# Performance work log

Hardware: AMD Instinct MI355X
Metric: run time of the kernel (lower is better)

Reference implementation:

```python
import jax, jax.numpy as jnp
import numpy as np

B, V, D, E, F, H, HD = 16, 1024, 16, 64, 16, 128, 64
GRAPH_LAYERS, FLOW_ITERS, DUAL_ITERS = 2, 10, 10
STEP, MOM, BIG = 0.01, 0.9, 1e9


def _build_graph():
    # circulant graph: node v's d-th out-neighbor is v + offs[d] (mod V); offsets paired (o, -o)
    offs = np.array([1, -1, 2, -2, 3, -3, 4, -4, 5, -5, 6, -6, 7, -7, 8, -8], dtype=np.int32)
    v = np.arange(V, dtype=np.int32)[:, None]
    d = np.broadcast_to(np.arange(D, dtype=np.int32)[None, :], (V, D))
    adj = ((v + offs[None, :]) % V).astype(np.int32)
    inv_adj = ((v - offs[None, :]) % V).astype(np.int32)
    in_idx = np.stack([inv_adj, d], axis=-1)    # d-th incoming edge of v == out-edge (inv_adj[v,d], slot d)
    rev_idx = np.stack([adj, d], axis=-1)       # out-edge (v,d) is the d-th incoming edge of adj[v,d]
    opp_idx = np.stack([adj, d ^ 1], axis=-1)   # opposite edge (w->v) is slot d^1 at w (paired offsets)
    bt = lambda x: jnp.asarray(np.broadcast_to(x[None], (B,) + x.shape).copy())
    return bt(adj), bt(inv_adj), bt(in_idx), bt(rev_idx), bt(opp_idx)


def setup_inputs() -> dict:
    key = jax.random.key(0)
    ks = jax.random.split(key, 16)
    adj_lst, inv_adj_lst, in_indices, rev_indices, opp_indices = _build_graph()
    rn = lambda k, shape, scale=1.0: jax.random.normal(k, shape, dtype=jnp.float32) * scale
    s = lambda fan: 1.0 / float(np.sqrt(fan))
    return {
        'demands': rn(ks[0], (B, V, 1)),
        'node_features': rn(ks[1], (B, V, F)),
        'edge_lengths': jax.random.uniform(ks[2], (B, V, D), dtype=jnp.float32),
        'norm_edge_lengths': jax.random.uniform(ks[3], (B, V, D), dtype=jnp.float32),
        'node_emb': rn(ks[4], (V, E)),
        'W_enc': rn(ks[5], (E + F, H), s(E + F)), 'b_enc': jnp.zeros((H,), jnp.float32),
        'W_gat': rn(ks[6], (H, H), s(H)), 'b_gat': jnp.zeros((H,), jnp.float32),
        'a_gat': rn(ks[7], (H,), s(H)),
        'W_gru_x': rn(ks[8], (H, 3 * H), s(H)), 'W_gru_h': rn(ks[9], (H, 3 * H), s(H)),
        'b_gru': jnp.zeros((3 * H,), jnp.float32),
        'W_dec1': rn(ks[10], (2 * H, HD), s(2 * H)), 'b_dec1': jnp.zeros((HD,), jnp.float32),
        'W_dec2': rn(ks[11], (HD, 1), s(HD)), 'b_dec2': jnp.zeros((1,), jnp.float32),
        'W_dual1': rn(ks[12], (H, HD), s(H)), 'b_dual1': jnp.zeros((HD,), jnp.float32),
        'W_dual2': rn(ks[13], (HD, 1), s(HD)), 'b_dual2': jnp.zeros((1,), jnp.float32),
        'adj_lst': adj_lst, 'inv_adj_lst': inv_adj_lst,
        'in_indices': in_indices, 'rev_indices': rev_indices, 'opp_indices': opp_indices,
        'num_nodes': jnp.full((B,), V, dtype=jnp.int32),
    }


def _gather_nodes(values, idx, valid):
    # masked_gather with set_zero=True: values (B,V,H), idx (B,V,D) -> (B,V,D,H)
    bb = jnp.arange(values.shape[0])[:, None, None]
    g = values[bb, jnp.clip(idx, 0, values.shape[1] - 1)]
    return g * valid[..., None]


def _gather_edges(x, idx):
    # gather_nd into a (B,V,D,...) tensor; idx (B,V,D,2) = (node, slot), batch implicit
    bb = jnp.arange(x.shape[0])[:, None, None]
    return x[bb, idx[..., 0], idx[..., 1]]


def _sparsemax(z):
    n = z.shape[-1]
    zs = jnp.sort(z, axis=-1)[..., ::-1]
    k = jnp.arange(1, n + 1, dtype=z.dtype)
    zc = jnp.cumsum(zs, axis=-1)
    support = (1.0 + k * zs) > zc
    kz = jnp.sum(support, axis=-1, keepdims=True)
    tau = (jnp.take_along_axis(zc, kz - 1, axis=-1) - 1.0) / kz.astype(z.dtype)
    return jnp.maximum(z - tau, 0.0)


def _forward(demands, node_features, edge_lengths, norm_edge_lengths, node_emb, W_enc, b_enc,
             W_gat, b_gat, a_gat, W_gru_x, W_gru_h, b_gru, W_dec1, b_dec1, W_dec2, b_dec2,
             W_dual1, b_dual1, W_dual2, b_dual2,
             adj_lst, inv_adj_lst, in_indices, rev_indices, opp_indices, num_nodes):
    f32 = jnp.float32
    # embedding lookup with max_norm=1
    nrm = jnp.linalg.norm(node_emb, axis=-1, keepdims=True)
    emb = node_emb / jnp.maximum(nrm, 1.0)
    emb_b = jnp.broadcast_to(emb[None], (demands.shape[0], V, E))
    node_enc = jnp.concatenate([emb_b, node_features], axis=-1) @ W_enc + b_enc   # (B,V,H)
    mask = (adj_lst == num_nodes[:, None, None]).astype(f32)                       # 1 = padded slot
    valid = 1.0 - mask
    initial = _gather_nodes(node_enc, adj_lst, valid)                              # (B,V,D,H)
    h = initial
    for _ in range(GRAPH_LAYERS):
        # DirectionalGAT: per-edge transform, masked attention over slots, directional regather
        t = jnp.tanh(h @ W_gat + b_gat)                                            # (B,V,D,H)
        logits = jnp.einsum('bvdh,h->bvd', t, a_gat) - BIG * mask
        attn = jax.nn.softmax(logits, axis=-1)
        node_msg = jnp.einsum('bvd,bvdh->bvh', attn, t)                            # (B,V,H)
        msg = _gather_nodes(node_msg, adj_lst, valid)
        x = jnp.tanh(msg + initial)
        # GRU cell, shared weights over all edge states
        gx = x @ W_gru_x + b_gru
        gh = h @ W_gru_h
        z = jax.nn.sigmoid(gx[..., :H] + gh[..., :H])
        r = jax.nn.sigmoid(gx[..., H:2 * H] + gh[..., H:2 * H])
        cand = jnp.tanh(gx[..., 2 * H:] + r * gh[..., 2 * H:])
        h = z * h + (1.0 - z) * cand
    # decoder over (encoding, encoding + opposite-edge encoding)
    comb = h + _gather_edges(h, opp_indices)
    dec_in = jnp.concatenate([h, comb], axis=-1)
    nw = (jnp.tanh(dec_in @ W_dec1 + b_dec1) @ W_dec2 + b_dec2)[..., 0]            # (B,V,D)
    # destination attention: normalize over incoming edges, map back to outgoing layout
    inv_mask = (inv_adj_lst == num_nodes[:, None, None]).astype(f32)
    in_w = _gather_edges(nw, in_indices)
    dest_attn = jax.nn.softmax(in_w - BIG * inv_mask, axis=-1)
    nw = _gather_edges(dest_attn, rev_indices)
    pred = nw - BIG * mask
    normalized = _sparsemax(pred) * valid
    # iterative proportional min-cost-flow solver
    def mcf_step(flow, _):
        inflow = jnp.sum(_gather_edges(flow, in_indices), axis=-1, keepdims=True)  # (B,V,1)
        return normalized * jax.nn.relu(inflow - demands), None
    flow, _ = jax.lax.scan(mcf_step, jnp.zeros_like(normalized), None, length=FLOW_ITERS)
    flow_cost = jnp.sum(flow * flow, axis=(1, 2))                                  # square cost fn
    # dual variables + dual flow (projected momentum gradient descent)
    node_states = jnp.sum(h, axis=2)                                               # (B,V,H)
    dual_vars = jax.nn.relu(jnp.tanh(node_states @ W_dual1 + b_dual1) @ W_dual2 + b_dual2)  # (B,V,1)
    dual = mask * dual_vars
    dual_tr = _gather_nodes(dual_vars, adj_lst, valid)[..., 0]
    dual_diff = dual_tr - dual                                                     # (B,V,D)
    def dual_step(carry, _):
        f, vel = carry
        grad = 2.0 * f + dual_diff                                                 # d/df [f^2 + dual_diff*f]
        vel = MOM * vel - STEP * grad
        f = jax.nn.relu(f + vel)
        return (f, vel), None
    (dual_flows, _), _ = jax.lax.scan(dual_step, (jnp.zeros_like(dual_diff), jnp.zeros_like(dual_diff)), None, length=DUAL_ITERS)
    dual_flows = dual_flows * valid
    dual_demand = jnp.sum(dual_vars * demands, axis=(1, 2))
    dual_cost = jnp.sum(dual_flows * dual_flows + dual_diff * dual_flows, axis=(1, 2)) - dual_demand
    return flow_cost - dual_cost                                                   # (B,) primal-dual gap loss


def reference(demands, node_features, edge_lengths, norm_edge_lengths, node_emb, W_enc, b_enc,
              W_gat, b_gat, a_gat, W_gru_x, W_gru_h, b_gru, W_dec1, b_dec1, W_dec2, b_dec2,
              W_dual1, b_dual1, W_dual2, b_dual2,
              adj_lst, inv_adj_lst, in_indices, rev_indices, opp_indices, num_nodes):
    return _forward(demands, node_features, edge_lengths, norm_edge_lengths, node_emb, W_enc, b_enc,
                    W_gat, b_gat, a_gat, W_gru_x, W_gru_h, b_gru, W_dec1, b_dec1, W_dec2, b_dec2,
                    W_dual1, b_dual1, W_dual2, b_dual2,
                    adj_lst, inv_adj_lst, in_indices, rev_indices, opp_indices, num_nodes)
```

## Files before the change

kernel.cpp:

```cpp
#include <hip/hip_runtime.h>
#include <hip/hip_bf16.h>

#define B 16
#define V 1024
#define D 16
#define E 64
#define F 16
#define H 128
#define HD 64
#define BV (B*V)
#define BVD (B*V*D)

#define OFF_HNB      0
#define OFF_NORM     (OFF_HNB + BV*H/2)
#define OFF_DV       (OFF_NORM + BVD)
#define OFF_WT       (OFF_DV + BV)
#define OFF_WTG      (OFF_WT + 65536)
#define OFF_WPQ      (OFF_WTG + 8192)
#define OFF_WU1T     (OFF_WPQ + 8192)
#define OFF_WENCT    (OFF_WU1T + 4096)

typedef __attribute__((ext_vector_type(8))) short bf16x8;
typedef __attribute__((ext_vector_type(4))) float f32x4;

__device__ __forceinline__ short f2bf(float f){
  __hip_bfloat16 b = __float2bfloat16(f);
  return *reinterpret_cast<short*>(&b);
}
__device__ __forceinline__ float bf2f(short s){
  __hip_bfloat16 b; *reinterpret_cast<short*>(&b) = s;
  return __bfloat162float(b);
}
__device__ __forceinline__ float frcp(float x){ return __builtin_amdgcn_rcpf(x); }
__device__ __forceinline__ float fsig(float x){ return frcp(1.f + __expf(-x)); }
__device__ __forceinline__ float ftanh(float x){
  float e = __expf(-2.f*fabsf(x));
  float r = (1.f - e)*frcp(1.f + e);
  return copysignf(r, x);
}

__global__ __launch_bounds__(256) void k_pre(const float* __restrict__ Wx, const float* __restrict__ Wh,
    const float* __restrict__ Wg, const float* __restrict__ W1, const float* __restrict__ Wu1,
    const float* __restrict__ Wenc,
    short* __restrict__ Wt, short* __restrict__ Wgt, short* __restrict__ Wpq,
    short* __restrict__ Wu1t, short* __restrict__ Wenct){
  int bid = blockIdx.x, tid = threadIdx.x;
  if (bid < 512){
    int n = bid, k = tid;
    int g = n >> 7, j = n & 127;
    float v;
    if (g == 0)      v = (k < 128) ? Wx[k*384 + j]       : Wh[(k-128)*384 + j];
    else if (g == 1) v = (k < 128) ? Wx[k*384 + 128 + j] : Wh[(k-128)*384 + 128 + j];
    else if (g == 2) v = (k < 128) ? Wx[k*384 + 256 + j] : 0.f;
    else             v = (k < 128) ? 0.f                 : Wh[(k-128)*384 + 256 + j];
    Wt[n*256 + k] = f2bf(v);
    return;
  }
  if (bid < 576){
    int idx = (bid-512)*256 + tid;
    int n = idx >> 7, k = idx & 127;
    Wgt[n*128 + k] = f2bf(Wg[k*128 + n]);
    return;
  }
  if (bid < 608){
    int idx = (bid-576)*256 + tid;
    int n = idx >> 7, k = idx & 127;
    float wb = W1[(k+128)*HD + n];
    float wa = W1[k*HD + n];
    Wpq[n*128 + k]      = f2bf(wa + wb);
    Wpq[(64+n)*128 + k] = f2bf(wb);
    return;
  }
  if (bid < 640){
    int idx = (bid-608)*256 + tid;
    int n = idx >> 7, k = idx & 127;
    Wu1t[n*128 + k] = f2bf(Wu1[k*HD + n]);
    return;
  }
  {
    int nn = (bid-640)*2 + (tid >> 7);
    int kk = tid & 127;
    if (kk < 96) Wenct[nn*96 + kk] = f2bf(kk < 80 ? Wenc[kk*128 + nn] : 0.f);
  }
}

__global__ __launch_bounds__(256) void k_mega(const float* __restrict__ emb, const float* __restrict__ nf,
    const short* __restrict__ Wenct, const float* __restrict__ benc, const int* __restrict__ adj,
    const short* __restrict__ Wgt, const float* __restrict__ bg, const float* __restrict__ ag,
    const short* __restrict__ Wt, const float* __restrict__ bgru, short* __restrict__ hout){
  __shared__ short NE[96][136];
  __shared__ short T[96][136];
  __shared__ short H1[80][136];
  __shared__ short X[80][136];
  __shared__ float Lp[4][96];
  __shared__ float Ls[96];
  __shared__ float nrmv[96];
  short (*As)[104] = reinterpret_cast<short(*)[104]>(&H1[0][0]);

  int tid = threadIdx.x;
  int blk = blockIdx.x;
  int b = blk >> 4;
  int n0 = (blk & 15) << 6;
  int w = tid >> 6, lane = tid & 63;
  int l15 = lane & 15, quad = lane >> 4;

  if (tid < 96){
    int v = (n0 - 16 + tid) & 1023;
    const float4* e4 = reinterpret_cast<const float4*>(&emb[v*E]);
    float ss = 0.f;
    #pragma unroll
    for (int q=0;q<16;q++){ float4 x = e4[q]; ss += x.x*x.x + x.y*x.y + x.z*x.z + x.w*x.w; }
    nrmv[tid] = frcp(fmaxf(sqrtf(ss), 1.f));
  }
  __syncthreads();
  for (int e=tid; e<96*16; e+=256){
    int r = e >> 4, q = e & 15;
    int v = (n0 - 16 + r) & 1023;
    float4 x = reinterpret_cast<const float4*>(&emb[v*E])[q];
    float iv = nrmv[r];
    short4 s; s.x=f2bf(x.x*iv); s.y=f2bf(x.y*iv); s.z=f2bf(x.z*iv); s.w=f2bf(x.w*iv);
    *reinterpret_cast<short4*>(&As[r][q*4]) = s;
  }
  for (int e=tid; e<96*4; e+=256){
    int r = e >> 2, q = e & 3;
    int m = (b<<10) + ((n0 - 16 + r) & 1023);
    float4 x = reinterpret_cast<const float4*>(&nf[(long)m*F])[q];
    short4 s; s.x=f2bf(x.x); s.y=f2bf(x.y); s.z=f2bf(x.z); s.w=f2bf(x.w);
    *reinterpret_cast<short4*>(&As[r][64 + q*4]) = s;
    short4 z; z.x=0; z.y=0; z.z=0; z.w=0;
    *reinterpret_cast<short4*>(&As[r][80 + q*4]) = z;
  }
  __syncthreads();
  {
    f32x4 acc[6][2];
    #pragma unroll
    for (int mt=0;mt<6;mt++)
      #pragma unroll
      for (int u=0;u<2;u++) acc[mt][u] = (f32x4){0.f,0.f,0.f,0.f};
    #pragma unroll
    for (int kc=0;kc<3;kc++){
      int k0 = kc*32;
      bf16x8 a[6];
      #pragma unroll
      for (int mt=0;mt<6;mt++)
        a[mt] = *reinterpret_cast<const bf16x8*>(&As[16*mt + l15][k0 + quad*8]);
      #pragma unroll
      for (int u=0;u<2;u++){
        bf16x8 bfr = *reinterpret_cast<const bf16x8*>(&Wenct[(32*w + 16*u + l15)*96 + k0 + quad*8]);
        #pragma unroll
        for (int mt=0;mt<6;mt++)
          acc[mt][u] = __builtin_amdgcn_mfma_f32_16x16x32_bf16(a[mt], bfr, acc[mt][u], 0,0,0);
      }
    }
    #pragma unroll
    for (int u=0;u<2;u++){
      int c = 32*w + 16*u + l15;
      float bb = benc[c];
      #pragma unroll
      for (int mt=0;mt<6;mt++)
        #pragma unroll
        for (int reg=0;reg<4;reg++)
          NE[16*mt + quad*4 + reg][c] = f2bf(acc[mt][u][reg] + bb);
    }
  }
  __syncthreads();
  {
    f32x4 acc[6][2];
    #pragma unroll
    for (int mt=0;mt<6;mt++)
      #pragma unroll
      for (int u=0;u<2;u++) acc[mt][u] = (f32x4){0.f,0.f,0.f,0.f};
    #pragma unroll
    for (int kc=0;kc<4;kc++){
      int k0 = kc*32;
      bf16x8 a[6];
      #pragma unroll
      for (int mt=0;mt<6;mt++)
        a[mt] = *reinterpret_cast<const bf16x8*>(&NE[16*mt + l15][k0 + quad*8]);
      #pragma unroll
      for (int u=0;u<2;u++){
        bf16x8 bfr = *reinterpret_cast<const bf16x8*>(&Wgt[(32*w + 16*u + l15)*128 + k0 + quad*8]);
        #pragma unroll
        for (int mt=0;mt<6;mt++)
          acc[mt][u] = __builtin_amdgcn_mfma_f32_16x16x32_bf16(a[mt], bfr, acc[mt][u], 0,0,0);
      }
    }
    float lp[6][4];
    #pragma unroll
    for (int mt=0;mt<6;mt++)
      #pragma unroll
      for (int reg=0;reg<4;reg++) lp[mt][reg] = 0.f;
    #pragma unroll
    for (int u=0;u<2;u++){
      int c = 32*w + 16*u + l15;
      float bgc = bg[c], agc = ag[c];
      #pragma unroll
      for (int mt=0;mt<6;mt++){
        #pragma unroll
        for (int reg=0;reg<4;reg++){
          float t = ftanh(acc[mt][u][reg] + bgc);
          T[16*mt + quad*4 + reg][c] = f2bf(t);
          lp[mt][reg] += t * agc;
        }
      }
    }
    #pragma unroll
    for (int mt=0;mt<6;mt++)
      #pragma unroll
      for (int reg=0;reg<4;reg++){
        lp[mt][reg] += __shfl_xor(lp[mt][reg], 1);
        lp[mt][reg] += __shfl_xor(lp[mt][reg], 2);
        lp[mt][reg] += __shfl_xor(lp[mt][reg], 4);
        lp[mt][reg] += __shfl_xor(lp[mt][reg], 8);
      }
    if (l15 == 0){
      #pragma unroll
      for (int mt=0;mt<6;mt++)
        #pragma unroll
        for (int reg=0;reg<4;reg++)
          Lp[w][16*mt + quad*4 + reg] = lp[mt][reg];
    }
  }
  __syncthreads();
  if (tid < 96) Ls[tid] = Lp[0][tid]+Lp[1][tid]+Lp[2][tid]+Lp[3][tid];
  __syncthreads();
  for (int e=tid; e<320; e+=256){
    int vl = e >> 2, seg = e & 3;
    int wg = (b<<10) + ((n0 - 8 + vl) & 1023);
    int li[16]; float at[16];
    float m = -1e30f;
    #pragma unroll
    for (int d=0; d<16; d++){
      int a = adj[wg*16 + d];
      li[d] = (a - n0 + 16) & 1023;
      m = fmaxf(m, Ls[li[d]]);
    }
    float s = 0.f;
    #pragma unroll
    for (int d=0; d<16; d++){ at[d] = __expf(Ls[li[d]] - m); s += at[d]; }
    float inv = frcp(s);
    #pragma unroll
    for (int d=0; d<16; d++) at[d] *= inv;
    #pragma unroll
    for (int c8=0; c8<4; c8++){
      int c = seg*32 + c8*8;
      float acc8[8] = {0,0,0,0,0,0,0,0};
      #pragma unroll 4
      for (int d=0; d<16; d++){
        bf16x8 tv = *reinterpret_cast<const bf16x8*>(&T[li[d]][c]);
        float a = at[d];
        #pragma unroll
        for (int q=0;q<8;q++) acc8[q] += a * bf2f(tv[q]);
      }
      bf16x8 nv = *reinterpret_cast<const bf16x8*>(&NE[vl + 8][c]);
      bf16x8 xv;
      #pragma unroll
      for (int q=0;q<8;q++) xv[q] = f2bf(ftanh(acc8[q] + bf2f(nv[q])));
      *reinterpret_cast<bf16x8*>(&X[vl][c]) = xv;
    }
  }
  __syncthreads();
  {
    f32x4 acc[5][4][2];
    #pragma unroll
    for (int mt=0;mt<5;mt++)
      #pragma unroll
      for (int g=0;g<4;g++)
        #pragma unroll
        for (int u=0;u<2;u++) acc[mt][g][u] = (f32x4){0.f,0.f,0.f,0.f};
    for (int k8=0;k8<8;k8++){
      int k0 = k8*32;
      int gg = (k8 < 4) ? 2 : 3;
      bf16x8 a[5];
      #pragma unroll
      for (int mt=0;mt<5;mt++){
        if (k8 < 4) a[mt] = *reinterpret_cast<const bf16x8*>(&X[16*mt + l15][k0 + quad*8]);
        else        a[mt] = *reinterpret_cast<const bf16x8*>(&NE[16*mt + l15 + 8][k0 - 128 + quad*8]);
      }
      bf16x8 bz[2], br[2], bc[2];
      #pragma unroll
      for (int u=0;u<2;u++){
        int ncol = 32*w + 16*u + l15;
        int koff = k0 + quad*8;
        bz[u] = *reinterpret_cast<const bf16x8*>(&Wt[(ncol      )*256 + koff]);
        br[u] = *reinterpret_cast<const bf16x8*>(&Wt[(ncol + 128)*256 + koff]);
        bc[u] = *reinterpret_cast<const bf16x8*>(&Wt[(ncol + gg*128)*256 + koff]);
      }
      #pragma unroll
      for (int mt=0;mt<5;mt++){
        #pragma unroll
        for (int u=0;u<2;u++){
          acc[mt][0][u]  = __builtin_amdgcn_mfma_f32_16x16x32_bf16(a[mt], bz[u], acc[mt][0][u], 0,0,0);
          acc[mt][1][u]  = __builtin_amdgcn_mfma_f32_16x16x32_bf16(a[mt], br[u], acc[mt][1][u], 0,0,0);
          acc[mt][gg][u] = __builtin_amdgcn_mfma_f32_16x16x32_bf16(a[mt], bc[u], acc[mt][gg][u], 0,0,0);
        }
      }
    }
    #pragma unroll
    for (int u=0;u<2;u++){
      int j = 32*w + 16*u + l15;
      float bjz = bgru[j], bjr = bgru[128 + j], bjc = bgru[256 + j];
      #pragma unroll
      for (int mt=0;mt<5;mt++){
        #pragma unroll
        for (int reg=0;reg<4;reg++){
          int rl = 16*mt + quad*4 + reg;
          float z = fsig(acc[mt][0][u][reg] + bjz);
          float r = fsig(acc[mt][1][u][reg] + bjr);
          float cand = ftanh(acc[mt][2][u][reg] + bjc + r*acc[mt][3][u][reg]);
          float ho = bf2f(NE[rl + 8][j]);
          H1[rl][j] = f2bf(z*ho + (1.f - z)*cand);
        }
      }
    }
  }
  __syncthreads();
  {
    f32x4 acc[5][2];
    #pragma unroll
    for (int mt=0;mt<5;mt++)
      #pragma unroll
      for (int u=0;u<2;u++) acc[mt][u] = (f32x4){0.f,0.f,0.f,0.f};
    #pragma unroll
    for (int kc=0;kc<4;kc++){
      int k0 = kc*32;
      bf16x8 a[5];
      #pragma unroll
      for (int mt=0;mt<5;mt++)
        a[mt] = *reinterpret_cast<const bf16x8*>(&H1[16*mt + l15][k0 + quad*8]);
      #pragma unroll
      for (int u=0;u<2;u++){
        bf16x8 bfr = *reinterpret_cast<const bf16x8*>(&Wgt[(32*w + 16*u + l15)*128 + k0 + quad*8]);
        #pragma unroll
        for (int mt=0;mt<5;mt++)
          acc[mt][u] = __builtin_amdgcn_mfma_f32_16x16x32_bf16(a[mt], bfr, acc[mt][u], 0,0,0);
      }
    }
    float lp[5][4];
    #pragma unroll
    for (int mt=0;mt<5;mt++)
      #pragma unroll
      for (int reg=0;reg<4;reg++) lp[mt][reg] = 0.f;
    #pragma unroll
    for (int u=0;u<2;u++){
      int c = 32*w + 16*u + l15;
      float bgc = bg[c], agc = ag[c];
      #pragma unroll
      for (int mt=0;mt<5;mt++){
        #pragma unroll
        for (int reg=0;reg<4;reg++){
          float t = ftanh(acc[mt][u][reg] + bgc);
          T[16*mt + quad*4 + reg][c] = f2bf(t);
          lp[mt][reg] += t * agc;
        }
      }
    }
    #pragma unroll
    for (int mt=0;mt<5;mt++)
      #pragma unroll
      for (int reg=0;reg<4;reg++){
        lp[mt][reg] += __shfl_xor(lp[mt][reg], 1);
        lp[mt][reg] += __shfl_xor(lp[mt][reg], 2);
        lp[mt][reg] += __shfl_xor(lp[mt][reg], 4);
        lp[mt][reg] += __shfl_xor(lp[mt][reg], 8);
      }
    if (l15 == 0){
      #pragma unroll
      for (int mt=0;mt<5;mt++)
        #pragma unroll
        for (int reg=0;reg<4;reg++)
          Lp[w][16*mt + quad*4 + reg] = lp[mt][reg];
    }
  }
  __syncthreads();
  if (tid < 80) Ls[tid] = Lp[0][tid]+Lp[1][tid]+Lp[2][tid]+Lp[3][tid];
  __syncthreads();
  {
    int vl = tid >> 2, seg = tid & 3;
    int vg = (b<<10) + n0 + vl;
    int li[16]; float at[16];
    float m = -1e30f;
    #pragma unroll
    for (int d=0; d<16; d++){
      int a = adj[vg*16 + d];
      li[d] = (a - n0 + 8) & 1023;
      m = fmaxf(m, Ls[li[d]]);
    }
    float s = 0.f;
    #pragma unroll
    for (int d=0; d<16; d++){ at[d] = __expf(Ls[li[d]] - m); s += at[d]; }
    float inv = frcp(s);
    #pragma unroll
    for (int d=0; d<16; d++) at[d] *= inv;
    #pragma unroll
    for (int c8=0; c8<4; c8++){
      int c = seg*32 + c8*8;
      float acc8[8] = {0,0,0,0,0,0,0,0};
      #pragma unroll 4
      for (int d=0; d<16; d++){
        bf16x8 tv = *reinterpret_cast<const bf16x8*>(&T[li[d]][c]);
        float a = at[d];
        #pragma unroll
        for (int q=0;q<8;q++) acc8[q] += a * bf2f(tv[q]);
      }
      bf16x8 nv = *reinterpret_cast<const bf16x8*>(&NE[vl + 16][c]);
      bf16x8 xv;
      #pragma unroll
      for (int q=0;q<8;q++) xv[q] = f2bf(ftanh(acc8[q] + bf2f(nv[q])));
      *reinterpret_cast<bf16x8*>(&X[vl][c]) = xv;
    }
  }
  __syncthreads();
  {
    f32x4 acc[4][4][2];
    #pragma unroll
    for (int mt=0;mt<4;mt++)
      #pragma unroll
      for (int g=0;g<4;g++)
        #pragma unroll
        for (int u=0;u<2;u++) acc[mt][g][u] = (f32x4){0.f,0.f,0.f,0.f};
    for (int k8=0;k8<8;k8++){
      int k0 = k8*32;
      int gg = (k8 < 4) ? 2 : 3;
      bf16x8 a[4];
      #pragma unroll
      for (int mt=0;mt<4;mt++){
        if (k8 < 4) a[mt] = *reinterpret_cast<const bf16x8*>(&X[16*mt + l15][k0 + quad*8]);
        else        a[mt] = *reinterpret_cast<const bf16x8*>(&H1[16*mt + l15 + 8][k0 - 128 + quad*8]);
      }
      bf16x8 bz[2], br[2], bc[2];
      #pragma unroll
      for (int u=0;u<2;u++){
        int ncol = 32*w + 16*u + l15;
        int koff = k0 + quad*8;
        bz[u] = *reinterpret_cast<const bf16x8*>(&Wt[(ncol      )*256 + koff]);
        br[u] = *reinterpret_cast<const bf16x8*>(&Wt[(ncol + 128)*256 + koff]);
        bc[u] = *reinterpret_cast<const bf16x8*>(&Wt[(ncol + gg*128)*256 + koff]);
      }
      #pragma unroll
      for (int mt=0;mt<4;mt++){
        #pragma unroll
        for (int u=0;u<2;u++){
          acc[mt][0][u]  = __builtin_amdgcn_mfma_f32_16x16x32_bf16(a[mt], bz[u], acc[mt][0][u], 0,0,0);
          acc[mt][1][u]  = __builtin_amdgcn_mfma_f32_16x16x32_bf16(a[mt], br[u], acc[mt][1][u], 0,0,0);
          acc[mt][gg][u] = __builtin_amdgcn_mfma_f32_16x16x32_bf16(a[mt], bc[u], acc[mt][gg][u], 0,0,0);
        }
      }
    }
    __syncthreads();
    #pragma unroll
    for (int u=0;u<2;u++){
      int j = 32*w + 16*u + l15;
      float bjz = bgru[j], bjr = bgru[128 + j], bjc = bgru[256 + j];
      #pragma unroll
      for (int mt=0;mt<4;mt++){
        #pragma unroll
        for (int reg=0;reg<4;reg++){
          int rl = 16*mt + quad*4 + reg;
          float z = fsig(acc[mt][0][u][reg] + bjz);
          float r = fsig(acc[mt][1][u][reg] + bjr);
          float cand = ftanh(acc[mt][2][u][reg] + bjc + r*acc[mt][3][u][reg]);
          float ho = bf2f(H1[rl + 8][j]);
          X[rl][j] = f2bf(z*ho + (1.f - z)*cand);
        }
      }
    }
  }
  __syncthreads();
  for (int idx=tid; idx<64*16; idx+=256){
    int r = idx >> 4, c8 = idx & 15;
    *reinterpret_cast<bf16x8*>(&hout[(long)((b<<10) + n0 + r)*128 + c8*8]) =
        *reinterpret_cast<const bf16x8*>(&X[r][c8*8]);
  }
}

__global__ __launch_bounds__(256) void k_decdas(const short* __restrict__ hn, const int* __restrict__ adj,
    const int* __restrict__ invadj, const short* __restrict__ Wpq, const float* __restrict__ b1,
    const float* __restrict__ W2, const float* __restrict__ b2_,
    const short* __restrict__ Wu1t, const float* __restrict__ bu1, const float* __restrict__ Wu2,
    const float* __restrict__ bu2_, float* __restrict__ norm_, float* __restrict__ dv){
  __shared__ short Hs[112][136];
  __shared__ short PQb[112][132];
  __shared__ short NSs[64][136];
  __shared__ int adjL[64][16];
  __shared__ float dvp[64][4];
  __shared__ float b1s[64], w2s[64], bu1s[64], wu2s[64];
  int tid = threadIdx.x;
  int blk = blockIdx.x;
  int b = blk >> 4;
  int n0 = (blk & 15) << 6;
  if (tid < 64){ b1s[tid] = b1[tid]; w2s[tid] = W2[tid]; bu1s[tid] = bu1[tid]; wu2s[tid] = Wu2[tid]; }
  for (int idx=tid; idx<112*16; idx+=256){
    int r = idx >> 4, c8 = idx & 15;
    int g = (b << 10) + ((n0 - 24 + r) & 1023);
    *reinterpret_cast<bf16x8*>(&Hs[r][c8*8]) =
        *reinterpret_cast<const bf16x8*>(&hn[(long)g*128 + c8*8]);
  }
  #pragma unroll
  for (int e=0;e<4;e++){
    int idx = e*256 + tid;
    int r = idx >> 4, d = idx & 15;
    int a = adj[((b<<10) + n0 + r)*16 + d];
    adjL[r][d] = (a - n0 + 24) & 1023;
  }
  __syncthreads();
  int w = tid >> 6, lane = tid & 63;
  int l15 = lane & 15, quad = lane >> 4;
  {
    f32x4 acc[7][2];
    #pragma unroll
    for (int mt=0;mt<7;mt++)
      #pragma unroll
      for (int u=0;u<2;u++) acc[mt][u] = (f32x4){0.f,0.f,0.f,0.f};
    #pragma unroll
    for (int kc=0;kc<4;kc++){
      int k0 = kc*32;
      bf16x8 a[7];
      #pragma unroll
      for (int mt=0;mt<7;mt++)
        a[mt] = *reinterpret_cast<const bf16x8*>(&Hs[16*mt + l15][k0 + quad*8]);
      #pragma unroll
      for (int u=0;u<2;u++){
        bf16x8 bfr = *reinterpret_cast<const bf16x8*>(&Wpq[(32*w + 16*u + l15)*128 + k0 + quad*8]);
        #pragma unroll
        for (int mt=0;mt<7;mt++)
          acc[mt][u] = __builtin_amdgcn_mfma_f32_16x16x32_bf16(a[mt], bfr, acc[mt][u], 0,0,0);
      }
    }
    #pragma unroll
    for (int u=0;u<2;u++){
      int c = 32*w + 16*u + l15;
      #pragma unroll
      for (int mt=0;mt<7;mt++)
        #pragma unroll
        for (int reg=0;reg<4;reg++)
          PQb[16*mt + quad*4 + reg][c] = f2bf(acc[mt][u][reg]);
    }
  }
  #pragma unroll
  for (int e=0;e<4;e++){
    int idx = e*256 + tid;
    int r = idx >> 4, c8 = idx & 15;
    float acc8[8] = {0,0,0,0,0,0,0,0};
    #pragma unroll 4
    for (int d=0; d<16; d++){
      bf16x8 hv = *reinterpret_cast<const bf16x8*>(&Hs[adjL[r][d]][c8*8]);
      #pragma unroll
      for (int q=0;q<8;q++) acc8[q] += bf2f(hv[q]);
    }
    bf16x8 sv;
    #pragma unroll
    for (int q=0;q<8;q++) sv[q] = f2bf(acc8[q]);
    *reinterpret_cast<bf16x8*>(&NSs[r][c8*8]) = sv;
  }
  __syncthreads();
  {
    f32x4 acc[4];
    #pragma unroll
    for (int mt=0;mt<4;mt++) acc[mt] = (f32x4){0.f,0.f,0.f,0.f};
    #pragma unroll
    for (int kc=0;kc<4;kc++){
      int k0 = kc*32;
      bf16x8 bfr = *reinterpret_cast<const bf16x8*>(&Wu1t[(16*w + l15)*128 + k0 + quad*8]);
      #pragma unroll
      for (int mt=0;mt<4;mt++){
        bf16x8 a = *reinterpret_cast<const bf16x8*>(&NSs[16*mt + l15][k0 + quad*8]);
        acc[mt] = __builtin_amdgcn_mfma_f32_16x16x32_bf16(a, bfr, acc[mt], 0,0,0);
      }
    }
    int n = 16*w + l15;
    float bn = bu1s[n], wn = wu2s[n];
    #pragma unroll
    for (int mt=0;mt<4;mt++){
      #pragma unroll
      for (int reg=0;reg<4;reg++){
        float p = ftanh(acc[mt][reg] + bn) * wn;
        p += __shfl_xor(p, 1);
        p += __shfl_xor(p, 2);
        p += __shfl_xor(p, 4);
        p += __shfl_xor(p, 8);
        if (l15 == 0) dvp[16*mt + quad*4 + reg][w] = p;
      }
    }
  }
  __syncthreads();
  float* nws = reinterpret_cast<float*>(&Hs[0][0]);
  float b2v = b2_[0];
  for (int e = tid; e < 96*16; e += 256){
    int rr = e >> 4, d = e & 15;
    int wnode = (n0 + rr - 16) & 1023;
    int wg = (b<<10) + wnode;
    int a = adj[wg*16 + d];
    int al = (a - n0 + 24) & 1023;
    int wl = rr + 8;
    float p = 0.f;
    #pragma unroll 8
    for (int c=0;c<64;c++)
      p += ftanh(bf2f(PQb[al][c]) + bf2f(PQb[wl][64 + c]) + b1s[c]) * w2s[c];
    nws[rr*17 + d] = p + b2v;
  }
  __syncthreads();
  if (tid < 64){
    float val = dvp[tid][0]+dvp[tid][1]+dvp[tid][2]+dvp[tid][3];
    dv[(b<<10) + n0 + tid] = fmaxf(val + bu2_[0], 0.f);
  }
  float* datt = reinterpret_cast<float*>(&PQb[0][0]);
  if (tid < 80){
    int wnode = (n0 + tid - 8) & 1023;
    int wg = (b<<10) + wnode;
    float vals[16];
    float m = -1e30f;
    #pragma unroll
    for (int d=0; d<16; d++){
      int iv = invadj[wg*16 + d];
      int il = (iv - n0 + 16) & 1023;
      vals[d] = nws[il*17 + d];
      m = fmaxf(m, vals[d]);
    }
    float s = 0.f;
    #pragma unroll
    for (int d=0; d<16; d++){ vals[d] = __expf(vals[d]-m); s += vals[d]; }
    float inv = frcp(s);
    #pragma unroll
    for (int d=0; d<16; d++) datt[tid*17 + d] = vals[d]*inv;
  }
  __syncthreads();
  if (tid < 64){
    int vg = (b<<10) + n0 + tid;
    float z[16], s[16];
    #pragma unroll
    for (int d=0; d<16; d++){
      int al = adjL[tid][d] - 16;
      z[d] = datt[al*17 + d];
      s[d] = z[d];
    }
    #pragma unroll
    for (int k2 = 2; k2 <= 16; k2 <<= 1){
      #pragma unroll
      for (int jj = k2 >> 1; jj > 0; jj >>= 1){
        #pragma unroll
        for (int i = 0; i < 16; i++){
          int l = i ^ jj;
          if (l > i){
            bool up = ((i & k2) == 0);
            float a = s[i], bb = s[l];
            bool sw = up ? (a > bb) : (a < bb);
            if (sw){ s[i]=bb; s[l]=a; }
          }
        }
      }
    }
    float cs = 0.f, zcs = 0.f; int kz = 1;
    #pragma unroll
    for (int j=0;j<16;j++){
      float zj = s[15-j];
      cs += zj;
      if (1.f + (float)(j+1)*zj > cs){ kz = j+1; zcs = cs; }
    }
    float tau = (zcs - 1.f)/(float)kz;
    #pragma unroll
    for (int d=0; d<16; d++) norm_[(long)vg*16 + d] = fmaxf(z[d]-tau, 0.f);
  }
}

__global__ __launch_bounds__(1024) void k_flowfin(const float* __restrict__ norm_,
    const float* __restrict__ dem, const int* __restrict__ invadj, const float* __restrict__ dv,
    float* __restrict__ out){
  __shared__ float nrmS[V*17];
  __shared__ float sbuf[2][V];
  __shared__ float r1[16], r2[16], r3[16];
  int b = blockIdx.x, v = threadIdx.x;
  int gv = (b<<10) + v;
  {
    const float4* src = reinterpret_cast<const float4*>(&norm_[(long)gv*16]);
    #pragma unroll
    for (int q4=0; q4<4; q4++){
      float4 x = src[q4];
      nrmS[v*17 + q4*4+0] = x.x; nrmS[v*17 + q4*4+1] = x.y;
      nrmS[v*17 + q4*4+2] = x.z; nrmS[v*17 + q4*4+3] = x.w;
    }
  }
  int iv[16];
  #pragma unroll
  for (int d4=0; d4<4; d4++){
    int4 i4 = reinterpret_cast<const int4*>(&invadj[(long)gv*16])[d4];
    iv[d4*4+0]=i4.x; iv[d4*4+1]=i4.y; iv[d4*4+2]=i4.z; iv[d4*4+3]=i4.w;
  }
  float dm = dem[gv];
  sbuf[0][v] = 0.f;
  __syncthreads();
  float nrg[16]; float nr2 = 0.f;
  #pragma unroll
  for (int d=0; d<16; d++){
    nrg[d] = nrmS[iv[d]*17 + d];
    float nv = nrmS[v*17 + d];
    nr2 += nv*nv;
  }
  int p = 0;
  float s = 0.f;
  for (int it=0; it<10; it++){
    float inflow = 0.f;
    #pragma unroll
    for (int d=0; d<16; d++) inflow += nrg[d]*sbuf[p][iv[d]];
    s = fmaxf(inflow - dm, 0.f);
    sbuf[1-p][v] = s;
    p ^= 1;
    __syncthreads();
  }
  float partF = nr2 * s * s;
  float dvv = dv[gv];
  float f = 0.f, vel = 0.f;
  #pragma unroll
  for (int it=0; it<10; it++){
    float g = 2.f*f + dvv;
    vel = 0.9f*vel - 0.01f*g;
    f = fmaxf(f + vel, 0.f);
  }
  float partD = f*f + dvv*f;
  float partDD = dvv * dm;
  #pragma unroll
  for (int off=32; off>0; off>>=1){
    partF  += __shfl_down(partF, off);
    partD  += __shfl_down(partD, off);
    partDD += __shfl_down(partDD, off);
  }
  if ((v & 63) == 0){ r1[v>>6] = partF; r2[v>>6] = partD; r3[v>>6] = partDD; }
  __syncthreads();
  if (v == 0){
    float sf = 0.f, sd = 0.f, sdd = 0.f;
    #pragma unroll
    for (int i=0;i<16;i++){ sf += r1[i]; sd += r2[i]; sdd += r3[i]; }
    out[b] = sf - (16.f*sd - sdd);
  }
}

extern "C" void kernel_launch(void* const* d_in, const int* in_sizes, int n_in,
                              void* d_out, int out_size, void* d_ws, size_t ws_size,
                              hipStream_t stream){
  (void)in_sizes; (void)n_in; (void)out_size; (void)ws_size;
  const float* demands = (const float*)d_in[0];
  const float* nf      = (const float*)d_in[1];
  const float* emb     = (const float*)d_in[4];
  const float* Wenc    = (const float*)d_in[5];
  const float* benc    = (const float*)d_in[6];
  const float* Wgat    = (const float*)d_in[7];
  const float* bgat    = (const float*)d_in[8];
  const float* agat    = (const float*)d_in[9];
  const float* Wgx     = (const float*)d_in[10];
  const float* Wgh     = (const float*)d_in[11];
  const float* bgru    = (const float*)d_in[12];
  const float* Wd1     = (const float*)d_in[13];
  const float* bd1     = (const float*)d_in[14];
  const float* Wd2     = (const float*)d_in[15];
  const float* bd2     = (const float*)d_in[16];
  const float* Wu1     = (const float*)d_in[17];
  const float* bu1     = (const float*)d_in[18];
  const float* Wu2     = (const float*)d_in[19];
  const float* bu2     = (const float*)d_in[20];
  const int* adj       = (const int*)d_in[21];
  const int* invadj    = (const int*)d_in[22];

  float* ws    = (float*)d_ws;
  short* hnB   = (short*)(ws + OFF_HNB);
  float* nrm   = ws + OFF_NORM;
  float* dv    = ws + OFF_DV;
  short* wt    = (short*)(ws + OFF_WT);
  short* wtg   = (short*)(ws + OFF_WTG);
  short* wpq   = (short*)(ws + OFF_WPQ);
  short* wu1t  = (short*)(ws + OFF_WU1T);
  short* wenct = (short*)(ws + OFF_WENCT);

  k_pre<<<704, 256, 0, stream>>>(Wgx, Wgh, Wgat, Wd1, Wu1, Wenc, wt, wtg, wpq, wu1t, wenct);
  k_mega<<<BV/64, 256, 0, stream>>>(emb, nf, wenct, benc, adj, wtg, bgat, agat, wt, bgru, hnB);
  k_decdas<<<BV/64, 256, 0, stream>>>(hnB, adj, invadj, wpq, bd1, Wd2, bd2,
                                      wu1t, bu1, Wu2, bu2, nrm, dv);
  k_flowfin<<<B, 1024, 0, stream>>>(nrm, demands, invadj, dv, (float*)d_out);
}
```

Before: 201.9 us.

## Double block size to 512 threads, splitting MFMA output columns across eight waves

k_mega and k_decdas move from 256 to 512 threads per block. Each of the eight waves now owns 16 output columns instead of 32 in every MFMA GEMM stage, and the elementwise loops and attention-logit partial reductions are re-strided or widened to match. The aim is more waves per CU to hide LDS and global latency, since the grid is only 256 blocks. In exchange, each wave reuses each A fragment across fewer B tiles, so LDS A-reads per MFMA double, and some stages leave waves idle (the wu1 GEMM runs only on waves 0-3).

```diff
diff --git a/kernel.cpp b/kernel.cpp
--- a/kernel.cpp
+++ b/kernel.cpp
@@ -84,7 +84,7 @@
   }
 }
 
-__global__ __launch_bounds__(256) void k_mega(const float* __restrict__ emb, const float* __restrict__ nf,
+__global__ __launch_bounds__(512,2) void k_mega(const float* __restrict__ emb, const float* __restrict__ nf,
     const short* __restrict__ Wenct, const float* __restrict__ benc, const int* __restrict__ adj,
     const short* __restrict__ Wgt, const float* __restrict__ bg, const float* __restrict__ ag,
     const short* __restrict__ Wt, const float* __restrict__ bgru, short* __restrict__ hout){
@@ -92,7 +92,7 @@
   __shared__ short T[96][136];
   __shared__ short H1[80][136];
   __shared__ short X[80][136];
-  __shared__ float Lp[4][96];
+  __shared__ float Lp[8][96];
   __shared__ float Ls[96];
   __shared__ float nrmv[96];
   short (*As)[104] = reinterpret_cast<short(*)[104]>(&H1[0][0]);
@@ -113,7 +113,7 @@
     nrmv[tid] = frcp(fmaxf(sqrtf(ss), 1.f));
   }
   __syncthreads();
-  for (int e=tid; e<96*16; e+=256){
+  for (int e=tid; e<96*16; e+=512){
     int r = e >> 4, q = e & 15;
     int v = (n0 - 16 + r) & 1023;
     float4 x = reinterpret_cast<const float4*>(&emb[v*E])[q];
@@ -121,7 +121,7 @@
     short4 s; s.x=f2bf(x.x*iv); s.y=f2bf(x.y*iv); s.z=f2bf(x.z*iv); s.w=f2bf(x.w*iv);
     *reinterpret_cast<short4*>(&As[r][q*4]) = s;
   }
-  for (int e=tid; e<96*4; e+=256){
+  for (int e=tid; e<96*4; e+=512){
     int r = e >> 2, q = e & 3;
     int m = (b<<10) + ((n0 - 16 + r) & 1023);
     float4 x = reinterpret_cast<const float4*>(&nf[(long)m*F])[q];
@@ -132,78 +132,53 @@
   }
   __syncthreads();
   {
-    f32x4 acc[6][2];
-    #pragma unroll
-    for (int mt=0;mt<6;mt++)
-      #pragma unroll
-      for (int u=0;u<2;u++) acc[mt][u] = (f32x4){0.f,0.f,0.f,0.f};
+    f32x4 acc[6];
+    #pragma unroll
+    for (int mt=0;mt<6;mt++) acc[mt] = (f32x4){0.f,0.f,0.f,0.f};
     #pragma unroll
     for (int kc=0;kc<3;kc++){
       int k0 = kc*32;
-      bf16x8 a[6];
-      #pragma unroll
-      for (int mt=0;mt<6;mt++)
-        a[mt] = *reinterpret_cast<const bf16x8*>(&As[16*mt + l15][k0 + quad*8]);
-      #pragma unroll
-      for (int u=0;u<2;u++){
-        bf16x8 bfr = *reinterpret_cast<const bf16x8*>(&Wenct[(32*w + 16*u + l15)*96 + k0 + quad*8]);
-        #pragma unroll
-        for (int mt=0;mt<6;mt++)
-          acc[mt][u] = __builtin_amdgcn_mfma_f32_16x16x32_bf16(a[mt], bfr, acc[mt][u], 0,0,0);
-      }
-    }
-    #pragma unroll
-    for (int u=0;u<2;u++){
-      int c = 32*w + 16*u + l15;
-      float bb = benc[c];
-      #pragma unroll
-      for (int mt=0;mt<6;mt++)
-        #pragma unroll
-        for (int reg=0;reg<4;reg++)
-          NE[16*mt + quad*4 + reg][c] = f2bf(acc[mt][u][reg] + bb);
-    }
+      bf16x8 bfr = *reinterpret_cast<const bf16x8*>(&Wenct[(16*w + l15)*96 + k0 + quad*8]);
+      #pragma unroll
+      for (int mt=0;mt<6;mt++){
+        bf16x8 a = *reinterpret_cast<const bf16x8*>(&As[16*mt + l15][k0 + quad*8]);
+        acc[mt] = __builtin_amdgcn_mfma_f32_16x16x32_bf16(a, bfr, acc[mt], 0,0,0);
+      }
+    }
+    int c = 16*w + l15;
+    float bb = benc[c];
+    #pragma unroll
+    for (int mt=0;mt<6;mt++)
+      #pragma unroll
+      for (int reg=0;reg<4;reg++)
+        NE[16*mt + quad*4 + reg][c] = f2bf(acc[mt][reg] + bb);
   }
   __syncthreads();
   {
-    f32x4 acc[6][2];
-    #pragma unroll
-    for (int mt=0;mt<6;mt++)
-      #pragma unroll
-      for (int u=0;u<2;u++) acc[mt][u] = (f32x4){0.f,0.f,0.f,0.f};
+    f32x4 acc[6];
+    #pragma unroll
+    for (int mt=0;mt<6;mt++) acc[mt] = (f32x4){0.f,0.f,0.f,0.f};
     #pragma unroll
     for (int kc=0;kc<4;kc++){
       int k0 = kc*32;
-      bf16x8 a[6];
-      #pragma unroll
-      for (int mt=0;mt<6;mt++)
-        a[mt] = *reinterpret_cast<const bf16x8*>(&NE[16*mt + l15][k0 + quad*8]);
-      #pragma unroll
-      for (int u=0;u<2;u++){
-        bf16x8 bfr = *reinterpret_cast<const bf16x8*>(&Wgt[(32*w + 16*u + l15)*128 + k0 + quad*8]);
-        #pragma unroll
-        for (int mt=0;mt<6;mt++)
-          acc[mt][u] = __builtin_amdgcn_mfma_f32_16x16x32_bf16(a[mt], bfr, acc[mt][u], 0,0,0);
-      }
-    }
+      bf16x8 bfr = *reinterpret_cast<const bf16x8*>(&Wgt[(16*w + l15)*128 + k0 + quad*8]);
+      #pragma unroll
+      for (int mt=0;mt<6;mt++){
+        bf16x8 a = *reinterpret_cast<const bf16x8*>(&NE[16*mt + l15][k0 + quad*8]);
+        acc[mt] = __builtin_amdgcn_mfma_f32_16x16x32_bf16(a, bfr, acc[mt], 0,0,0);
+      }
+    }
+    int c = 16*w + l15;
+    float bgc = bg[c], agc = ag[c];
     float lp[6][4];
     #pragma unroll
     for (int mt=0;mt<6;mt++)
       #pragma unroll
-      for (int reg=0;reg<4;reg++) lp[mt][reg] = 0.f;
-    #pragma unroll
-    for (int u=0;u<2;u++){
-      int c = 32*w + 16*u + l15;
-      float bgc = bg[c], agc = ag[c];
-      #pragma unroll
-      for (int mt=0;mt<6;mt++){
-        #pragma unroll
-        for (int reg=0;reg<4;reg++){
-          float t = ftanh(acc[mt][u][reg] + bgc);
-          T[16*mt + quad*4 + reg][c] = f2bf(t);
-          lp[mt][reg] += t * agc;
-        }
-      }
-    }
+      for (int reg=0;reg<4;reg++){
+        float t = ftanh(acc[mt][reg] + bgc);
+        T[16*mt + quad*4 + reg][c] = f2bf(t);
+        lp[mt][reg] = t * agc;
+      }
     #pragma unroll
     for (int mt=0;mt<6;mt++)
       #pragma unroll
@@ -222,10 +197,15 @@
     }
   }
   __syncthreads();
-  if (tid < 96) Ls[tid] = Lp[0][tid]+Lp[1][tid]+Lp[2][tid]+Lp[3][tid];
-  __syncthreads();
-  for (int e=tid; e<320; e+=256){
-    int vl = e >> 2, seg = e & 3;
+  if (tid < 96){
+    float s = 0.f;
+    #pragma unroll
+    for (int i=0;i<8;i++) s += Lp[i][tid];
+    Ls[tid] = s;
+  }
+  __syncthreads();
+  if (tid < 320){
+    int vl = tid >> 2, seg = tid & 3;
     int wg = (b<<10) + ((n0 - 8 + vl) & 1023);
     int li[16]; float at[16];
     float m = -1e30f;
@@ -261,100 +241,70 @@
   }
   __syncthreads();
   {
-    f32x4 acc[5][4][2];
+    f32x4 acc[5][4];
     #pragma unroll
     for (int mt=0;mt<5;mt++)
       #pragma unroll
-      for (int g=0;g<4;g++)
-        #pragma unroll
-        for (int u=0;u<2;u++) acc[mt][g][u] = (f32x4){0.f,0.f,0.f,0.f};
+      for (int g=0;g<4;g++) acc[mt][g] = (f32x4){0.f,0.f,0.f,0.f};
     for (int k8=0;k8<8;k8++){
       int k0 = k8*32;
       int gg = (k8 < 4) ? 2 : 3;
-      bf16x8 a[5];
+      int ncol = 16*w + l15;
+      int koff = k0 + quad*8;
+      bf16x8 bz = *reinterpret_cast<const bf16x8*>(&Wt[(ncol      )*256 + koff]);
+      bf16x8 br = *reinterpret_cast<const bf16x8*>(&Wt[(ncol + 128)*256 + koff]);
+      bf16x8 bc = *reinterpret_cast<const bf16x8*>(&Wt[(ncol + gg*128)*256 + koff]);
       #pragma unroll
       for (int mt=0;mt<5;mt++){
-        if (k8 < 4) a[mt] = *reinterpret_cast<const bf16x8*>(&X[16*mt + l15][k0 + quad*8]);
-        else        a[mt] = *reinterpret_cast<const bf16x8*>(&NE[16*mt + l15 + 8][k0 - 128 + quad*8]);
-      }
-      bf16x8 bz[2], br[2], bc[2];
-      #pragma unroll
-      for (int u=0;u<2;u++){
-        int ncol = 32*w + 16*u + l15;
-        int koff = k0 + quad*8;
-        bz[u] = *reinterpret_cast<const bf16x8*>(&Wt[(ncol      )*256 + koff]);
-        br[u] = *reinterpret_cast<const bf16x8*>(&Wt[(ncol + 128)*256 + koff]);
-        bc[u] = *reinterpret_cast<const bf16x8*>(&Wt[(ncol + gg*128)*256 + koff]);
-      }
-      #pragma unroll
-      for (int mt=0;mt<5;mt++){
-        #pragma unroll
-        for (int u=0;u<2;u++){
-          acc[mt][0][u]  = __builtin_amdgcn_mfma_f32_16x16x32_bf16(a[mt], bz[u], acc[mt][0][u], 0,0,0);
-          acc[mt][1][u]  = __builtin_amdgcn_mfma_f32_16x16x32_bf16(a[mt], br[u], acc[mt][1][u], 0,0,0);
-          acc[mt][gg][u] = __builtin_amdgcn_mfma_f32_16x16x32_bf16(a[mt], bc[u], acc[mt][gg][u], 0,0,0);
-        }
-      }
-    }
-    #pragma unroll
-    for (int u=0;u<2;u++){
-      int j = 32*w + 16*u + l15;
-      float bjz = bgru[j], bjr = bgru[128 + j], bjc = bgru[256 + j];
-      #pragma unroll
-      for (int mt=0;mt<5;mt++){
-        #pragma unroll
-        for (int reg=0;reg<4;reg++){
-          int rl = 16*mt + quad*4 + reg;
-          float z = fsig(acc[mt][0][u][reg] + bjz);
-          float r = fsig(acc[mt][1][u][reg] + bjr);
-          float cand = ftanh(acc[mt][2][u][reg] + bjc + r*acc[mt][3][u][reg]);
-          float ho = bf2f(NE[rl + 8][j]);
-          H1[rl][j] = f2bf(z*ho + (1.f - z)*cand);
-        }
+        bf16x8 a;
+        if (k8 < 4) a = *reinterpret_cast<const bf16x8*>(&X[16*mt + l15][k0 + quad*8]);
+        else        a = *reinterpret_cast<const bf16x8*>(&NE[16*mt + l15 + 8][k0 - 128 + quad*8]);
+        acc[mt][0]  = __builtin_amdgcn_mfma_f32_16x16x32_bf16(a, bz, acc[mt][0], 0,0,0);
+        acc[mt][1]  = __builtin_amdgcn_mfma_f32_16x16x32_bf16(a, br, acc[mt][1], 0,0,0);
+        acc[mt][gg] = __builtin_amdgcn_mfma_f32_16x16x32_bf16(a, bc, acc[mt][gg], 0,0,0);
+      }
+    }
+    int j = 16*w + l15;
+    float bjz = bgru[j], bjr = bgru[128 + j], bjc = bgru[256 + j];
+    #pragma unroll
+    for (int mt=0;mt<5;mt++){
+      #pragma unroll
+      for (int reg=0;reg<4;reg++){
+        int rl = 16*mt + quad*4 + reg;
+        float z = fsig(acc[mt][0][reg] + bjz);
+        float r = fsig(acc[mt][1][reg] + bjr);
+        float cand = ftanh(acc[mt][2][reg] + bjc + r*acc[mt][3][reg]);
+        float ho = bf2f(NE[rl + 8][j]);
+        H1[rl][j] = f2bf(z*ho + (1.f - z)*cand);
       }
     }
   }
   __syncthreads();
   {
-    f32x4 acc[5][2];
-    #pragma unroll
-    for (int mt=0;mt<5;mt++)
-      #pragma unroll
-      for (int u=0;u<2;u++) acc[mt][u] = (f32x4){0.f,0.f,0.f,0.f};
+    f32x4 acc[5];
+    #pragma unroll
+    for (int mt=0;mt<5;mt++) acc[mt] = (f32x4){0.f,0.f,0.f,0.f};
     #pragma unroll
     for (int kc=0;kc<4;kc++){
       int k0 = kc*32;
-      bf16x8 a[5];
-      #pragma unroll
-      for (int mt=0;mt<5;mt++)
-        a[mt] = *reinterpret_cast<const bf16x8*>(&H1[16*mt + l15][k0 + quad*8]);
-      #pragma unroll
-      for (int u=0;u<2;u++){
-        bf16x8 bfr = *reinterpret_cast<const bf16x8*>(&Wgt[(32*w + 16*u + l15)*128 + k0 + quad*8]);
-        #pragma unroll
-        for (int mt=0;mt<5;mt++)
-          acc[mt][u] = __builtin_amdgcn_mfma_f32_16x16x32_bf16(a[mt], bfr, acc[mt][u], 0,0,0);
-      }
-    }
+      bf16x8 bfr = *reinterpret_cast<const bf16x8*>(&Wgt[(16*w + l15)*128 + k0 + quad*8]);
+      #pragma unroll
+      for (int mt=0;mt<5;mt++){
+        bf16x8 a = *reinterpret_cast<const bf16x8*>(&H1[16*mt + l15][k0 + quad*8]);
+        acc[mt] = __builtin_amdgcn_mfma_f32_16x16x32_bf16(a, bfr, acc[mt], 0,0,0);
+      }
+    }
+    int c = 16*w + l15;
+    float bgc = bg[c], agc = ag[c];
     float lp[5][4];
     #pragma unroll
     for (int mt=0;mt<5;mt++)
       #pragma unroll
-      for (int reg=0;reg<4;reg++) lp[mt][reg] = 0.f;
-    #pragma unroll
-    for (int u=0;u<2;u++){
-      int c = 32*w + 16*u + l15;
-      float bgc = bg[c], agc = ag[c];
-      #pragma unroll
-      for (int mt=0;mt<5;mt++){
-        #pragma unroll
-        for (int reg=0;reg<4;reg++){
-          float t = ftanh(acc[mt][u][reg] + bgc);
-          T[16*mt + quad*4 + reg][c] = f2bf(t);
-          lp[mt][reg] += t * agc;
-        }
-      }
-    }
+      for (int reg=0;reg<4;reg++){
+        float t = ftanh(acc[mt][reg] + bgc);
+        T[16*mt + quad*4 + reg][c] = f2bf(t);
+        lp[mt][reg] = t * agc;
+      }
     #pragma unroll
     for (int mt=0;mt<5;mt++)
       #pragma unroll
@@ -373,9 +323,14 @@
     }
   }
   __syncthreads();
-  if (tid < 80) Ls[tid] = Lp[0][tid]+Lp[1][tid]+Lp[2][tid]+Lp[3][tid];
-  __syncthreads();
-  {
+  if (tid < 80){
+    float s = 0.f;
+    #pragma unroll
+    for (int i=0;i<8;i++) s += Lp[i][tid];
+    Ls[tid] = s;
+  }
+  __syncthreads();
+  if (tid < 256){
     int vl = tid >> 2, seg = tid & 3;
     int vg = (b<<10) + n0 + vl;
     int li[16]; float at[16];
@@ -412,69 +367,54 @@
   }
   __syncthreads();
   {
-    f32x4 acc[4][4][2];
+    f32x4 acc[4][4];
     #pragma unroll
     for (int mt=0;mt<4;mt++)
       #pragma unroll
-      for (int g=0;g<4;g++)
-        #pragma unroll
-        for (int u=0;u<2;u++) acc[mt][g][u] = (f32x4){0.f,0.f,0.f,0.f};
+      for (int g=0;g<4;g++) acc[mt][g] = (f32x4){0.f,0.f,0.f,0.f};
     for (int k8=0;k8<8;k8++){
       int k0 = k8*32;
       int gg = (k8 < 4) ? 2 : 3;
-      bf16x8 a[4];
+      int ncol = 16*w + l15;
+      int koff = k0 + quad*8;
+      bf16x8 bz = *reinterpret_cast<const bf16x8*>(&Wt[(ncol      )*256 + koff]);
+      bf16x8 br = *reinterpret_cast<const bf16x8*>(&Wt[(ncol + 128)*256 + koff]);
+      bf16x8 bc = *reinterpret_cast<const bf16x8*>(&Wt[(ncol + gg*128)*256 + koff]);
       #pragma unroll
       for (int mt=0;mt<4;mt++){
-        if (k8 < 4) a[mt] = *reinterpret_cast<const bf16x8*>(&X[16*mt + l15][k0 + quad*8]);
-        else        a[mt] = *reinterpret_cast<const bf16x8*>(&H1[16*mt + l15 + 8][k0 - 128 + quad*8]);
-      }
-      bf16x8 bz[2], br[2], bc[2];
-      #pragma unroll
-      for (int u=0;u<2;u++){
-        int ncol = 32*w + 16*u + l15;
-        int koff = k0 + quad*8;
-        bz[u] = *reinterpret_cast<const bf16x8*>(&Wt[(ncol      )*256 + koff]);
-        br[u] = *reinterpret_cast<const bf16x8*>(&Wt[(ncol + 128)*256 + koff]);
-        bc[u] = *reinterpret_cast<const bf16x8*>(&Wt[(ncol + gg*128)*256 + koff]);
-      }
-      #pragma unroll
-      for (int mt=0;mt<4;mt++){
-        #pragma unroll
-        for (int u=0;u<2;u++){
-          acc[mt][0][u]  = __builtin_amdgcn_mfma_f32_16x16x32_bf16(a[mt], bz[u], acc[mt][0][u], 0,0,0);
-          acc[mt][1][u]  = __builtin_amdgcn_mfma_f32_16x16x32_bf16(a[mt], br[u], acc[mt][1][u], 0,0,0);
-          acc[mt][gg][u] = __builtin_amdgcn_mfma_f32_16x16x32_bf16(a[mt], bc[u], acc[mt][gg][u], 0,0,0);
-        }
+        bf16x8 a;
+        if (k8 < 4) a = *reinterpret_cast<const bf16x8*>(&X[16*mt + l15][k0 + quad*8]);
+        else        a = *reinterpret_cast<const bf16x8*>(&H1[16*mt + l15 + 8][k0 - 128 + quad*8]);
+        acc[mt][0]  = __builtin_amdgcn_mfma_f32_16x16x32_bf16(a, bz, acc[mt][0], 0,0,0);
+        acc[mt][1]  = __builtin_amdgcn_mfma_f32_16x16x32_bf16(a, br, acc[mt][1], 0,0,0);
+        acc[mt][gg] = __builtin_amdgcn_mfma_f32_16x16x32_bf16(a, bc, acc[mt][gg], 0,0,0);
       }
     }
     __syncthreads();
-    #pragma unroll
-    for (int u=0;u<2;u++){
-      int j = 32*w + 16*u + l15;
-      float bjz = bgru[j], bjr = bgru[128 + j], bjc = bgru[256 + j];
-      #pragma unroll
-      for (int mt=0;mt<4;mt++){
-        #pragma unroll
-        for (int reg=0;reg<4;reg++){
-          int rl = 16*mt + quad*4 + reg;
-          float z = fsig(acc[mt][0][u][reg] + bjz);
-          float r = fsig(acc[mt][1][u][reg] + bjr);
-          float cand = ftanh(acc[mt][2][u][reg] + bjc + r*acc[mt][3][u][reg]);
-          float ho = bf2f(H1[rl + 8][j]);
-          X[rl][j] = f2bf(z*ho + (1.f - z)*cand);
-        }
-      }
-    }
-  }
-  __syncthreads();
-  for (int idx=tid; idx<64*16; idx+=256){
+    int j = 16*w + l15;
+    float bjz = bgru[j], bjr = bgru[128 + j], bjc = bgru[256 + j];
+    #pragma unroll
+    for (int mt=0;mt<4;mt++){
+      #pragma unroll
+      for (int reg=0;reg<4;reg++){
+        int rl = 16*mt + quad*4 + reg;
+        float z = fsig(acc[mt][0][reg] + bjz);
+        float r = fsig(acc[mt][1][reg] + bjr);
+        float cand = ftanh(acc[mt][2][reg] + bjc + r*acc[mt][3][reg]);
+        float ho = bf2f(H1[rl + 8][j]);
+        X[rl][j] = f2bf(z*ho + (1.f - z)*cand);
+      }
+    }
+  }
+  __syncthreads();
+  for (int idx=tid; idx<64*16; idx+=512){
     int r = idx >> 4, c8 = idx & 15;
     *reinterpret_cast<bf16x8*>(&hout[(long)((b<<10) + n0 + r)*128 + c8*8]) =
         *reinterpret_cast<const bf16x8*>(&X[r][c8*8]);
   }
 }
 
-__global__ __launch_bounds__(256) void k_decdas(const short* __restrict__ hn, const int* __restrict__ adj,
+__global__ __launch_bounds__(512,2) void k_decdas(const short* __restrict__ hn, const int* __restrict__ adj,
     const int* __restrict__ invadj, const short* __restrict__ Wpq, const float* __restrict__ b1,
     const float* __restrict__ W2, const float* __restrict__ b2_,
     const short* __restrict__ Wu1t, const float* __restrict__ bu1, const float* __restrict__ Wu2,
@@ -490,15 +430,13 @@
   int b = blk >> 4;
   int n0 = (blk & 15) << 6;
   if (tid < 64){ b1s[tid] = b1[tid]; w2s[tid] = W2[tid]; bu1s[tid] = bu1[tid]; wu2s[tid] = Wu2[tid]; }
-  for (int idx=tid; idx<112*16; idx+=256){
+  for (int idx=tid; idx<112*16; idx+=512){
     int r = idx >> 4, c8 = idx & 15;
     int g = (b << 10) + ((n0 - 24 + r) & 1023);
     *reinterpret_cast<bf16x8*>(&Hs[r][c8*8]) =
         *reinterpret_cast<const bf16x8*>(&hn[(long)g*128 + c8*8]);
   }
-  #pragma unroll
-  for (int e=0;e<4;e++){
-    int idx = e*256 + tid;
+  for (int idx=tid; idx<1024; idx+=512){
     int r = idx >> 4, d = idx & 15;
     int a = adj[((b<<10) + n0 + r)*16 + d];
     adjL[r][d] = (a - n0 + 24) & 1023;
@@ -507,39 +445,27 @@
   int w = tid >> 6, lane = tid & 63;
   int l15 = lane & 15, quad = lane >> 4;
   {
-    f32x4 acc[7][2];
-    #pragma unroll
-    for (int mt=0;mt<7;mt++)
-      #pragma unroll
-      for (int u=0;u<2;u++) acc[mt][u] = (f32x4){0.f,0.f,0.f,0.f};
+    f32x4 acc[7];
+    #pragma unroll
+    for (int mt=0;mt<7;mt++) acc[mt] = (f32x4){0.f,0.f,0.f,0.f};
     #pragma unroll
     for (int kc=0;kc<4;kc++){
       int k0 = kc*32;
-      bf16x8 a[7];
-      #pragma unroll
-      for (int mt=0;mt<7;mt++)
-        a[mt] = *reinterpret_cast<const bf16x8*>(&Hs[16*mt + l15][k0 + quad*8]);
-      #pragma unroll
-      for (int u=0;u<2;u++){
-        bf16x8 bfr = *reinterpret_cast<const bf16x8*>(&Wpq[(32*w + 16*u + l15)*128 + k0 + quad*8]);
-        #pragma unroll
-        for (int mt=0;mt<7;mt++)
-          acc[mt][u] = __builtin_amdgcn_mfma_f32_16x16x32_bf16(a[mt], bfr, acc[mt][u], 0,0,0);
-      }
-    }
-    #pragma unroll
-    for (int u=0;u<2;u++){
-      int c = 32*w + 16*u + l15;
-      #pragma unroll
-      for (int mt=0;mt<7;mt++)
-        #pragma unroll
-        for (int reg=0;reg<4;reg++)
-          PQb[16*mt + quad*4 + reg][c] = f2bf(acc[mt][u][reg]);
-    }
-  }
-  #pragma unroll
-  for (int e=0;e<4;e++){
-    int idx = e*256 + tid;
+      bf16x8 bfr = *reinterpret_cast<const bf16x8*>(&Wpq[(16*w + l15)*128 + k0 + quad*8]);
+      #pragma unroll
+      for (int mt=0;mt<7;mt++){
+        bf16x8 a = *reinterpret_cast<const bf16x8*>(&Hs[16*mt + l15][k0 + quad*8]);
+        acc[mt] = __builtin_amdgcn_mfma_f32_16x16x32_bf16(a, bfr, acc[mt], 0,0,0);
+      }
+    }
+    int c = 16*w + l15;
+    #pragma unroll
+    for (int mt=0;mt<7;mt++)
+      #pragma unroll
+      for (int reg=0;reg<4;reg++)
+        PQb[16*mt + quad*4 + reg][c] = f2bf(acc[mt][reg]);
+  }
+  for (int idx=tid; idx<64*16; idx+=512){
     int r = idx >> 4, c8 = idx & 15;
     float acc8[8] = {0,0,0,0,0,0,0,0};
     #pragma unroll 4
@@ -554,7 +480,7 @@
     *reinterpret_cast<bf16x8*>(&NSs[r][c8*8]) = sv;
   }
   __syncthreads();
-  {
+  if (w < 4){
     f32x4 acc[4];
     #pragma unroll
     for (int mt=0;mt<4;mt++) acc[mt] = (f32x4){0.f,0.f,0.f,0.f};
@@ -586,7 +512,7 @@
   __syncthreads();
   float* nws = reinterpret_cast<float*>(&Hs[0][0]);
   float b2v = b2_[0];
-  for (int e = tid; e < 96*16; e += 256){
+  for (int e = tid; e < 96*16; e += 512){
     int rr = e >> 4, d = e & 15;
     int wnode = (n0 + rr - 16) & 1023;
     int wg = (b<<10) + wnode;
@@ -771,8 +697,8 @@
   short* wenct = (short*)(ws + OFF_WENCT);
 
   k_pre<<<704, 256, 0, stream>>>(Wgx, Wgh, Wgat, Wd1, Wu1, Wenc, wt, wtg, wpq, wu1t, wenct);
-  k_mega<<<BV/64, 256, 0, stream>>>(emb, nf, wenct, benc, adj, wtg, bgat, agat, wt, bgru, hnB);
-  k_decdas<<<BV/64, 256, 0, stream>>>(hnB, adj, invadj, wpq, bd1, Wd2, bd2,
+  k_mega<<<BV/64, 512, 0, stream>>>(emb, nf, wenct, benc, adj, wtg, bgat, agat, wt, bgru, hnB);
+  k_decdas<<<BV/64, 512, 0, stream>>>(hnB, adj, invadj, wpq, bd1, Wd2, bd2,
                                       wu1t, bu1, Wu2, bu2, nrm, dv);
   k_flowfin<<<B, 1024, 0, stream>>>(nrm, demands, invadj, dv, (float*)d_out);
 }
```

New measurement: 184.8 us (median of 2 runs). 8.5% less time.
